# Performance work log

Measured on AMD Instinct MI355X. Metric: run time of the kernel, lower is better.

Reference implementation:

```python
import jax, jax.numpy as jnp
import numpy as np

N = 100000      # nodes
DEG = 16        # fixed out-degree per row of adj
E = N * DEG     # edges
IN_F, H_F, OUT_F = 64, 64, 64


def setup_inputs() -> dict:
    key = jax.random.key(0)
    k1, k2, k3, k4, k5, k6 = jax.random.split(key, 6)
    x = jax.random.normal(k1, (N, IN_F), dtype=jnp.float32)
    # fixed-degree graph: row i of adj has exactly DEG neighbors -> rowsum = DEG > 0
    dst = jnp.repeat(jnp.arange(N, dtype=jnp.int32), DEG)          # [E]
    src = jax.random.randint(k2, (E,), 0, N, dtype=jnp.int32)       # [E]
    # Linear params (torch nn.Linear: y = x @ W.T + b); store as [in, out]
    s1 = 1.0 / np.sqrt(2 * IN_F)
    s2 = 1.0 / np.sqrt(2 * H_F)
    W1 = jax.random.uniform(k3, (2 * IN_F, H_F), jnp.float32, -s1, s1)
    b1 = jax.random.uniform(k4, (H_F,), jnp.float32, -s1, s1)
    W2 = jax.random.uniform(k5, (2 * H_F, OUT_F), jnp.float32, -s2, s2)
    b2 = jax.random.uniform(k6, (OUT_F,), jnp.float32, -s2, s2)
    return {"x": x, "W1": W1, "b1": b1, "W2": W2, "b2": b2, "src": src, "dst": dst}


def _spmm_mean(h, src, dst, n_nodes):
    # row-normalized sparse adj @ h  == mean over neighbors (rows have DEG nbrs)
    deg = jax.ops.segment_sum(jnp.ones_like(src, dtype=h.dtype), dst, num_segments=n_nodes)
    w = (1.0 / jnp.maximum(deg, 1.0))[dst]                 # [E] edge weights 1/rowsum
    return jax.ops.segment_sum(h[src] * w[:, None], dst, num_segments=n_nodes)


def reference(x, W1, b1, W2, b2, src, dst):
    n = x.shape[0]
    h_neigh = _spmm_mean(x, src, dst, n)                   # [N, in]
    h = jnp.concatenate([x, h_neigh], axis=1)              # [N, 2*in]
    h = jax.nn.relu(h @ W1 + b1)                           # [N, h]
    h_neigh2 = _spmm_mean(h, src, dst, n)                  # [N, h]
    h2 = jnp.concatenate([h, h_neigh2], axis=1)            # [N, 2*h]
    return h2 @ W2 + b2                                    # [N, out]
```

## Files before the change

kernel.cpp:

```cpp
#include <hip/hip_runtime.h>


#define NN   100000
#define DEG  16
#define F    64
#define NPB  64
#define STR  65
#define JPW  16
#define EDG  (NN * DEG)

#if __has_builtin(__builtin_amdgcn_cvt_pk_f32_fp8) && __has_builtin(__builtin_amdgcn_cvt_pk_fp8_f32)
#define HW_FP8 1
#else
#define HW_FP8 0
#endif

typedef float v2f __attribute__((ext_vector_type(2)));

__device__ __forceinline__ ushort f2bf(float f) {
    unsigned u = __float_as_uint(f);
    return (ushort)((u + 0x7fffu + ((u >> 16) & 1u)) >> 16);
}
__device__ __forceinline__ float bf2f(ushort u) {
    return __uint_as_float(((unsigned)u) << 16);
}

#if !HW_FP8
__device__ __forceinline__ unsigned fp8_enc1(float f) {
    const unsigned u = __float_as_uint(f);
    const unsigned s = (u >> 31) << 7;
    const float af = fabsf(f);
    if (!(af < 448.f)) return s | 0x7E;
    if (af < 0.015625f) {
        const int n = (int)rintf(af * 512.f);
        return s | (unsigned)n;
    }
    unsigned au = u & 0x7FFFFFFFu;
    const unsigned lsb = (au >> 20) & 1u;
    au += 0x7FFFFu + lsb;
    const int e = (int)(au >> 23) - 127;
    if (e > 8) return s | 0x7E;
    return s | ((unsigned)(e + 7) << 3) | ((au >> 20) & 7u);
}
__device__ __forceinline__ float fp8_dec1(unsigned c) {
    const unsigned s = c >> 7;
    const int e = (int)((c >> 3) & 15u);
    const unsigned m = c & 7u;
    const float v = e ? ldexpf((float)(8 + m), e - 10) : ldexpf((float)m, -9);
    return s ? -v : v;
}
#endif

__device__ __forceinline__ unsigned fp8_pack4(float a, float b, float c, float d) {
#if HW_FP8
    int t = __builtin_amdgcn_cvt_pk_fp8_f32(a, b, 0, false);
    t     = __builtin_amdgcn_cvt_pk_fp8_f32(c, d, t, true);
    return (unsigned)t;
#else
    return fp8_enc1(a) | (fp8_enc1(b) << 8) | (fp8_enc1(c) << 16) | (fp8_enc1(d) << 24);
#endif
}

__device__ __forceinline__ void fp8_acc4(unsigned d, float* acc) {
#if HW_FP8
    const v2f lo = __builtin_amdgcn_cvt_pk_f32_fp8((int)d, false);
    const v2f hi = __builtin_amdgcn_cvt_pk_f32_fp8((int)d, true);
    acc[0] += lo.x; acc[1] += lo.y; acc[2] += hi.x; acc[3] += hi.y;
#else
    acc[0] += fp8_dec1(d & 0xffu);
    acc[1] += fp8_dec1((d >> 8) & 0xffu);
    acc[2] += fp8_dec1((d >> 16) & 0xffu);
    acc[3] += fp8_dec1(d >> 24);
#endif
}

__global__ __launch_bounds__(256)
void cvt_f32_fp8(const float* __restrict__ in, unsigned* __restrict__ out, int n4)
{
    int i = blockIdx.x * 256 + threadIdx.x;
    if (i < n4) {
        float4 v = ((const float4*)in)[i];
        out[i] = fp8_pack4(v.x, v.y, v.z, v.w);
    }
}

__device__ __forceinline__ void ce(unsigned& a, unsigned& b) {
    const unsigned lo = min(a, b), hi = max(a, b); a = lo; b = hi;
}
__device__ __forceinline__ void sort16(unsigned s[16]) {
    #pragma unroll
    for (int p = 1; p < 16; p <<= 1) {
        #pragma unroll
        for (int k = p; k >= 1; k >>= 1) {
            #pragma unroll
            for (int j = k & (p - 1); j + k < 16; j += 2 * k) {
                #pragma unroll
                for (int i = 0; i < k; ++i) {
                    if (i + j + k < 16)
                        if ((i + j) / (2 * p) == (i + j + k) / (2 * p))
                            ce(s[i + j], s[i + j + k]);
                }
            }
        }
    }
}

template<bool RELU, bool SELF_F32, bool EMIT_F32>
__global__ __launch_bounds__(256, 4)
void sage_fused(const float*  __restrict__ selfA,
                const ushort* __restrict__ selfB,
                const unsigned char* __restrict__ gat,
                const float*  __restrict__ W,
                const float*  __restrict__ bias,
                const int*    __restrict__ src,
                float*        __restrict__ out_f32,
                ushort*       __restrict__ out_bf16,
                unsigned char* __restrict__ out_fp8)
{
    __shared__ float    bufA[F][STR];
    __shared__ unsigned bufB[F / 2][STR];

    const int tid   = threadIdx.x;
    const int lane  = tid & 63;
    const int wave  = __builtin_amdgcn_readfirstlane(tid >> 6);
    const int node0 = blockIdx.x * NPB;

    #pragma unroll 4
    for (int m = 0; m < JPW; ++m) {
        const int n    = wave * JPW + m;
        const int node = node0 + n;
        float v = 0.f;
        if (node < NN)
            v = SELF_F32 ? selfA[(size_t)node * F + lane]
                         : bf2f(selfB[(size_t)node * F + lane]);
        bufA[lane][n] = v;
    }

    {
        const int q     = lane & 3;
        const int g     = lane >> 2;
        const int nloc  = wave * JPW + g;
        const int n     = node0 + nloc;
        const bool v    = n < NN;

        unsigned s[DEG];
        {
            const int4* p = (const int4*)(src + (size_t)n * DEG);
            #pragma unroll
            for (int t = 0; t < 4; ++t) {
                const int4 a = v ? p[t] : make_int4(0, 0, 0, 0);
                s[4*t+0] = a.x; s[4*t+1] = a.y;
                s[4*t+2] = a.z; s[4*t+3] = a.w;
            }
        }
        sort16(s);

        float a[16];
        #pragma unroll
        for (int f = 0; f < 16; ++f) a[f] = 0.f;

        #pragma unroll
        for (int e = 0; e < DEG; ++e) {
            const uint4 r = *(const uint4*)(gat + (size_t)s[e] * F + q * 16);
            fp8_acc4(r.x, a);
            fp8_acc4(r.y, a + 4);
            fp8_acc4(r.z, a + 8);
            fp8_acc4(r.w, a + 12);
        }

        #pragma unroll
        for (int t = 0; t < 8; ++t) {
            const unsigned d =
                (unsigned)f2bf(a[2*t]     * (1.0f / DEG)) |
                ((unsigned)f2bf(a[2*t+1]  * (1.0f / DEG)) << 16);
            bufB[8 * q + t][nloc] = d;
        }
    }
    __syncthreads();

    const int j0 = wave * JPW;
    float acc[JPW];
    #pragma unroll
    for (int j = 0; j < JPW; ++j) acc[j] = bias[j0 + j];

    #pragma unroll 4
    for (int k = 0; k < F; ++k) {
        const float v = bufA[k][lane];
        const float* Wr = W + k * F + j0;
        #pragma unroll
        for (int j = 0; j < JPW; ++j)
            acc[j] = fmaf(v, Wr[j], acc[j]);
    }
    #pragma unroll 2
    for (int kk = 0; kk < F / 2; ++kk) {
        const unsigned d = bufB[kk][lane];
        const float vlo = __uint_as_float(d << 16);
        const float vhi = __uint_as_float(d & 0xffff0000u);
        const float* Wlo = W + (F + 2 * kk)     * F + j0;
        const float* Whi = W + (F + 2 * kk + 1) * F + j0;
        #pragma unroll
        for (int j = 0; j < JPW; ++j) {
            acc[j] = fmaf(vlo, Wlo[j], acc[j]);
            acc[j] = fmaf(vhi, Whi[j], acc[j]);
        }
    }

    const int node = node0 + lane;
    if (node < NN) {
        if (RELU) {
            #pragma unroll
            for (int j = 0; j < JPW; ++j) acc[j] = fmaxf(acc[j], 0.f);
        }
        if (EMIT_F32) {
            float4* op = (float4*)(out_f32 + (size_t)node * F + j0);
            #pragma unroll
            for (int t = 0; t < 4; ++t)
                op[t] = make_float4(acc[4 * t], acc[4 * t + 1],
                                    acc[4 * t + 2], acc[4 * t + 3]);
        } else {
            uint4 q0, q1;
            #pragma unroll
            for (int t = 0; t < 8; ++t)
                (t < 4 ? (&q0.x)[t] : (&q1.x)[t - 4]) =
                    (unsigned)f2bf(acc[2 * t]) |
                    ((unsigned)f2bf(acc[2 * t + 1]) << 16);
            uint4* ob = (uint4*)(out_bf16 + (size_t)node * F + j0);
            ob[0] = q0; ob[1] = q1;

            uint4 p;
            #pragma unroll
            for (int t = 0; t < 4; ++t)
                (&p.x)[t] = fp8_pack4(acc[4*t], acc[4*t+1], acc[4*t+2], acc[4*t+3]);
            *(uint4*)(out_fp8 + (size_t)node * F + j0) = p;
        }
    }
}

template<bool RELU>
__global__ __launch_bounds__(256, 4)
void sage_layer_f32(const float* __restrict__ feat,
                    const float* __restrict__ W,
                    const float* __restrict__ bias,
                    const int*   __restrict__ src,
                    float*       __restrict__ out)
{
    __shared__ float buf[2 * F][STR];
    const int tid   = threadIdx.x;
    const int lane  = tid & 63;
    const int wave  = __builtin_amdgcn_readfirstlane(tid >> 6);
    const int node0 = blockIdx.x * NPB;

    #pragma unroll 2
    for (int m = 0; m < NPB / 4; ++m) {
        const int n    = wave * (NPB / 4) + m;
        const int node = node0 + n;
        if (node < NN) {
            buf[lane][n] = feat[node * F + lane];
            const int* sp = src + node * DEG;
            float s = 0.f;
            #pragma unroll
            for (int e = 0; e < DEG; ++e) s += feat[sp[e] * F + lane];
            buf[F + lane][n] = s * (1.0f / DEG);
        }
    }
    __syncthreads();

    const int j0 = wave * JPW;
    float acc[JPW];
    #pragma unroll
    for (int j = 0; j < JPW; ++j) acc[j] = bias[j0 + j];
    #pragma unroll 4
    for (int k = 0; k < 2 * F; ++k) {
        const float v = buf[k][lane];
        const float* Wr = W + k * F + j0;
        #pragma unroll
        for (int j = 0; j < JPW; ++j) acc[j] = fmaf(v, Wr[j], acc[j]);
    }
    const int node = node0 + lane;
    if (node < NN) {
        float4* op = (float4*)(out + node * F + j0);
        #pragma unroll
        for (int t = 0; t < 4; ++t) {
            float4 r = make_float4(acc[4 * t], acc[4 * t + 1],
                                   acc[4 * t + 2], acc[4 * t + 3]);
            if (RELU) {
                r.x = fmaxf(r.x, 0.f); r.y = fmaxf(r.y, 0.f);
                r.z = fmaxf(r.z, 0.f); r.w = fmaxf(r.w, 0.f);
            }
            op[t] = r;
        }
    }
}

extern "C" void kernel_launch(void* const* d_in, const int* in_sizes, int n_in,
                              void* d_out, int out_size, void* d_ws, size_t ws_size,
                              hipStream_t stream) {
    const float* x   = (const float*)d_in[0];
    const float* W1  = (const float*)d_in[1];
    const float* b1  = (const float*)d_in[2];
    const float* W2  = (const float*)d_in[3];
    const float* b2  = (const float*)d_in[4];
    const int*   src = (const int*)d_in[5];

    float* out = (float*)d_out;
    const int blocks = (NN + NPB - 1) / NPB;

    const size_t hFP8 = (size_t)NN * F;
    const size_t hBF  = (size_t)NN * F * sizeof(ushort);

    if (ws_size >= 2 * hFP8 + hBF) {
        unsigned char* x_fp8 = (unsigned char*)d_ws;
        ushort*        h_bf  = (ushort*)((char*)d_ws + hFP8);
        unsigned char* h_fp8 = (unsigned char*)d_ws + hFP8 + hBF;

        const int n4 = NN * F / 4;
        cvt_f32_fp8<<<(n4 + 255) / 256, 256, 0, stream>>>(x, (unsigned*)x_fp8, n4);
        sage_fused<true,  true,  false><<<blocks, 256, 0, stream>>>(
            x, nullptr, x_fp8, W1, b1, src, nullptr, h_bf, h_fp8);
        sage_fused<false, false, true ><<<blocks, 256, 0, stream>>>(
            nullptr, h_bf, h_fp8, W2, b2, src, out, nullptr, nullptr);
    } else {
        float* h = (float*)d_ws;
        sage_layer_f32<true ><<<blocks, 256, 0, stream>>>(x, W1, b1, src, h);
        sage_layer_f32<false><<<blocks, 256, 0, stream>>>(h, W2, b2, src, out);
    }
}
```

Measured before the change: 180.4 us.

## Use fp16 MFMA for SAGE layer matmuls with pre-packed weight fragments

Replaces the per-lane scalar FMA dense transform with 16x16x16 fp16 MFMA instructions. Weights are pre-packed into MFMA B-fragment layout by a new prep kernel. The self and aggregated features are staged in a swizzled fp16 LDS tile, and results go back through LDS to restore the row-per-lane output layout. The intermediate hidden state changes from bf16 to fp16, which alters precision and range, and the change adds an extra kernel launch and an extra LDS round trip.

```diff
diff --git a/kernel.cpp b/kernel.cpp
--- a/kernel.cpp
+++ b/kernel.cpp
@@ -8,6 +8,7 @@
 #define STR  65
 #define JPW  16
 #define EDG  (NN * DEG)
+#define OSTR 68
 
 #if __has_builtin(__builtin_amdgcn_cvt_pk_f32_fp8) && __has_builtin(__builtin_amdgcn_cvt_pk_fp8_f32)
 #define HW_FP8 1
@@ -16,14 +17,9 @@
 #endif
 
 typedef float v2f __attribute__((ext_vector_type(2)));
-
-__device__ __forceinline__ ushort f2bf(float f) {
-    unsigned u = __float_as_uint(f);
-    return (ushort)((u + 0x7fffu + ((u >> 16) & 1u)) >> 16);
-}
-__device__ __forceinline__ float bf2f(ushort u) {
-    return __uint_as_float(((unsigned)u) << 16);
-}
+typedef _Float16 f16x4 __attribute__((ext_vector_type(4)));
+typedef _Float16 f16x8 __attribute__((ext_vector_type(8)));
+typedef float f32x4 __attribute__((ext_vector_type(4)));
 
 #if !HW_FP8
 __device__ __forceinline__ unsigned fp8_enc1(float f) {
@@ -84,6 +80,24 @@
     }
 }
 
+__global__ __launch_bounds__(256)
+void prep_w(const float* __restrict__ W1, const float* __restrict__ W2,
+            _Float16* __restrict__ Wh)
+{
+    const int idx = blockIdx.x * 256 + threadIdx.x;
+    if (idx >= 4096) return;
+    const float* Wsrc = (idx >= 2048) ? W2 : W1;
+    const int rem = idx & 2047;
+    const int nt = rem >> 9, kt = (rem >> 6) & 7, l = rem & 63;
+    const int col = nt * 16 + (l & 15);
+    const int k0  = kt * 16 + (l >> 4) * 4;
+    f16x4 h;
+    #pragma unroll
+    for (int j = 0; j < 4; ++j)
+        h[j] = (_Float16)Wsrc[(size_t)(k0 + j) * F + col];
+    *(f16x4*)(Wh + (size_t)idx * 4) = h;
+}
+
 __device__ __forceinline__ void ce(unsigned& a, unsigned& b) {
     const unsigned lo = min(a, b), hi = max(a, b); a = lo; b = hi;
 }
@@ -105,35 +119,54 @@
     }
 }
 
+__device__ __forceinline__ int aChunk(int mt, int kt, int r, int sub) {
+    return (((((mt * 8 + kt) * 16 + r) << 2) | sub)) ^ ((kt & 3) << 2);
+}
+
 template<bool RELU, bool SELF_F32, bool EMIT_F32>
 __global__ __launch_bounds__(256, 4)
 void sage_fused(const float*  __restrict__ selfA,
-                const ushort* __restrict__ selfB,
+                const ushort* __restrict__ selfH,
                 const unsigned char* __restrict__ gat,
-                const float*  __restrict__ W,
+                const _Float16* __restrict__ Wf,
                 const float*  __restrict__ bias,
                 const int*    __restrict__ src,
                 float*        __restrict__ out_f32,
-                ushort*       __restrict__ out_bf16,
+                ushort*       __restrict__ out_h16,
                 unsigned char* __restrict__ out_fp8)
 {
-    __shared__ float    bufA[F][STR];
-    __shared__ unsigned bufB[F / 2][STR];
+    __shared__ __align__(16) unsigned char smem[NPB * OSTR * 4];
 
     const int tid   = threadIdx.x;
     const int lane  = tid & 63;
     const int wave  = __builtin_amdgcn_readfirstlane(tid >> 6);
     const int node0 = blockIdx.x * NPB;
 
-    #pragma unroll 4
-    for (int m = 0; m < JPW; ++m) {
-        const int n    = wave * JPW + m;
-        const int node = node0 + n;
-        float v = 0.f;
-        if (node < NN)
-            v = SELF_F32 ? selfA[(size_t)node * F + lane]
-                         : bf2f(selfB[(size_t)node * F + lane]);
-        bufA[lane][n] = v;
+    #pragma unroll
+    for (int m = 0; m < 2; ++m) {
+        const int c    = m * 4 + wave;
+        const int node = node0 + lane;
+        const int kt   = c >> 1, s2 = (c & 1) * 2;
+        const int boff = aChunk(lane >> 4, kt, lane & 15, s2) * 8;
+        if (SELF_F32) {
+            float4 v0 = make_float4(0.f, 0.f, 0.f, 0.f), v1 = v0;
+            if (node < NN) {
+                const float* p = selfA + (size_t)node * F + c * 8;
+                v0 = ((const float4*)p)[0];
+                v1 = ((const float4*)p)[1];
+            }
+            f16x8 h;
+            h[0] = (_Float16)v0.x; h[1] = (_Float16)v0.y;
+            h[2] = (_Float16)v0.z; h[3] = (_Float16)v0.w;
+            h[4] = (_Float16)v1.x; h[5] = (_Float16)v1.y;
+            h[6] = (_Float16)v1.z; h[7] = (_Float16)v1.w;
+            *(f16x8*)(smem + boff) = h;
+        } else {
+            uint4 v = make_uint4(0u, 0u, 0u, 0u);
+            if (node < NN)
+                v = *(const uint4*)(selfH + (size_t)node * F + c * 8);
+            *(uint4*)(smem + boff) = v;
+        }
     }
 
     {
@@ -168,69 +201,82 @@
             fp8_acc4(r.w, a + 12);
         }
 
+        const float sc = 1.0f / DEG;
+        f16x8 h0, h1;
         #pragma unroll
         for (int t = 0; t < 8; ++t) {
-            const unsigned d =
-                (unsigned)f2bf(a[2*t]     * (1.0f / DEG)) |
-                ((unsigned)f2bf(a[2*t+1]  * (1.0f / DEG)) << 16);
-            bufB[8 * q + t][nloc] = d;
-        }
+            h0[t] = (_Float16)(a[t]     * sc);
+            h1[t] = (_Float16)(a[8 + t] * sc);
+        }
+        const int kt = 4 + q;
+        *(f16x8*)(smem + aChunk(wave, kt, g, 0) * 8) = h0;
+        *(f16x8*)(smem + aChunk(wave, kt, g, 2) * 8) = h1;
     }
     __syncthreads();
 
     const int j0 = wave * JPW;
-    float acc[JPW];
-    #pragma unroll
-    for (int j = 0; j < JPW; ++j) acc[j] = bias[j0 + j];
-
-    #pragma unroll 4
-    for (int k = 0; k < F; ++k) {
-        const float v = bufA[k][lane];
-        const float* Wr = W + k * F + j0;
-        #pragma unroll
-        for (int j = 0; j < JPW; ++j)
-            acc[j] = fmaf(v, Wr[j], acc[j]);
-    }
-    #pragma unroll 2
-    for (int kk = 0; kk < F / 2; ++kk) {
-        const unsigned d = bufB[kk][lane];
-        const float vlo = __uint_as_float(d << 16);
-        const float vhi = __uint_as_float(d & 0xffff0000u);
-        const float* Wlo = W + (F + 2 * kk)     * F + j0;
-        const float* Whi = W + (F + 2 * kk + 1) * F + j0;
-        #pragma unroll
-        for (int j = 0; j < JPW; ++j) {
-            acc[j] = fmaf(vlo, Wlo[j], acc[j]);
-            acc[j] = fmaf(vhi, Whi[j], acc[j]);
-        }
+    const int lr = lane & 15, lq = lane >> 4;
+
+    f16x4 Wk[8];
+    #pragma unroll
+    for (int kt = 0; kt < 8; ++kt)
+        Wk[kt] = *(const f16x4*)(Wf + ((size_t)(wave * 8 + kt) * 64 + lane) * 4);
+
+    const float bv = bias[j0 + lr];
+    f32x4 acc[4];
+    #pragma unroll
+    for (int mt = 0; mt < 4; ++mt) acc[mt] = (f32x4){bv, bv, bv, bv};
+
+    #pragma unroll
+    for (int kt = 0; kt < 8; ++kt) {
+        #pragma unroll
+        for (int mt = 0; mt < 4; ++mt) {
+            const f16x4 af = *(const f16x4*)(smem + aChunk(mt, kt, lr, lq) * 8);
+            acc[mt] = __builtin_amdgcn_mfma_f32_16x16x16f16(af, Wk[kt], acc[mt], 0, 0, 0);
+        }
+    }
+    __syncthreads();
+
+    float* outS = (float*)smem;
+    #pragma unroll
+    for (int mt = 0; mt < 4; ++mt)
+        #pragma unroll
+        for (int p = 0; p < 4; ++p)
+            outS[(mt * 16 + lq * 4 + p) * OSTR + j0 + lr] = acc[mt][p];
+
+    float r[JPW];
+    #pragma unroll
+    for (int t = 0; t < 4; ++t) {
+        const float4 v = *(const float4*)(outS + lane * OSTR + j0 + 4 * t);
+        r[4*t+0] = v.x; r[4*t+1] = v.y; r[4*t+2] = v.z; r[4*t+3] = v.w;
     }
 
     const int node = node0 + lane;
     if (node < NN) {
         if (RELU) {
             #pragma unroll
-            for (int j = 0; j < JPW; ++j) acc[j] = fmaxf(acc[j], 0.f);
+            for (int j = 0; j < JPW; ++j) r[j] = fmaxf(r[j], 0.f);
         }
         if (EMIT_F32) {
             float4* op = (float4*)(out_f32 + (size_t)node * F + j0);
             #pragma unroll
             for (int t = 0; t < 4; ++t)
-                op[t] = make_float4(acc[4 * t], acc[4 * t + 1],
-                                    acc[4 * t + 2], acc[4 * t + 3]);
+                op[t] = make_float4(r[4 * t], r[4 * t + 1],
+                                    r[4 * t + 2], r[4 * t + 3]);
         } else {
-            uint4 q0, q1;
-            #pragma unroll
-            for (int t = 0; t < 8; ++t)
-                (t < 4 ? (&q0.x)[t] : (&q1.x)[t - 4]) =
-                    (unsigned)f2bf(acc[2 * t]) |
-                    ((unsigned)f2bf(acc[2 * t + 1]) << 16);
-            uint4* ob = (uint4*)(out_bf16 + (size_t)node * F + j0);
-            ob[0] = q0; ob[1] = q1;
+            f16x8 h0, h1;
+            #pragma unroll
+            for (int t = 0; t < 8; ++t) {
+                h0[t] = (_Float16)r[t];
+                h1[t] = (_Float16)r[8 + t];
+            }
+            *(f16x8*)(out_h16 + (size_t)node * F + j0)     = h0;
+            *(f16x8*)(out_h16 + (size_t)node * F + j0 + 8) = h1;
 
             uint4 p;
             #pragma unroll
             for (int t = 0; t < 4; ++t)
-                (&p.x)[t] = fp8_pack4(acc[4*t], acc[4*t+1], acc[4*t+2], acc[4*t+3]);
+                (&p.x)[t] = fp8_pack4(r[4*t], r[4*t+1], r[4*t+2], r[4*t+3]);
             *(uint4*)(out_fp8 + (size_t)node * F + j0) = p;
         }
     }
@@ -306,19 +352,22 @@
     const int blocks = (NN + NPB - 1) / NPB;
 
     const size_t hFP8 = (size_t)NN * F;
-    const size_t hBF  = (size_t)NN * F * sizeof(ushort);
-
-    if (ws_size >= 2 * hFP8 + hBF) {
+    const size_t hF16 = (size_t)NN * F * sizeof(ushort);
+    const size_t wTab = 2 * 8192 * sizeof(ushort);
+
+    if (ws_size >= 2 * hFP8 + hF16 + wTab) {
         unsigned char* x_fp8 = (unsigned char*)d_ws;
-        ushort*        h_bf  = (ushort*)((char*)d_ws + hFP8);
-        unsigned char* h_fp8 = (unsigned char*)d_ws + hFP8 + hBF;
+        ushort*        h_16  = (ushort*)((char*)d_ws + hFP8);
+        unsigned char* h_fp8 = (unsigned char*)d_ws + hFP8 + hF16;
+        _Float16*      Wh    = (_Float16*)((char*)d_ws + 2 * hFP8 + hF16);
 
         const int n4 = NN * F / 4;
         cvt_f32_fp8<<<(n4 + 255) / 256, 256, 0, stream>>>(x, (unsigned*)x_fp8, n4);
+        prep_w<<<16, 256, 0, stream>>>(W1, W2, Wh);
         sage_fused<true,  true,  false><<<blocks, 256, 0, stream>>>(
-            x, nullptr, x_fp8, W1, b1, src, nullptr, h_bf, h_fp8);
+            x, nullptr, x_fp8, Wh, b1, src, nullptr, h_16, h_fp8);
         sage_fused<false, false, true ><<<blocks, 256, 0, stream>>>(
-            nullptr, h_bf, h_fp8, W2, b2, src, out, nullptr, nullptr);
+            nullptr, h_16, h_fp8, Wh + 8192, b2, src, out, nullptr, nullptr);
     } else {
         float* h = (float*)d_ws;
         sage_layer_f32<true ><<<blocks, 256, 0, stream>>>(x, W1, b1, src, h);
```

Result: slower. 197.9 us (+9.7%).
